# Kernel optimization log

Measured on AMD Instinct MI355X. Metric: run time of the kernel, lower is better.

Reference implementation:

```python
import jax, jax.numpy as jnp
import numpy as np

NUM_TERMS = 3
HIDDEN = 64
CLAMP_MIN = 1e-10


def _hermite_basis(x, num_terms):
    hs = [jnp.ones_like(x)]
    if num_terms > 1:
        hs.append(2.0 * x)
    for n in range(1, num_terms - 1):
        hs.append(2.0 * x * hs[n] - 2.0 * n * hs[n - 1])
    return jnp.stack(hs[:num_terms], axis=-1)  # (..., num_terms)


def setup_inputs() -> dict:
    key = jax.random.key(0)
    ks = jax.random.split(key, 7)
    B, S = 2048, 1024
    ys_coeffs = jax.random.normal(ks[0], (B, S, 2), dtype=jnp.float32)
    # scoring MLP params: Linear(3,64) -> ReLU -> Linear(64,64) -> ReLU -> Linear(64,num_terms)
    def lin(k, fan_in, fan_out):
        bound = 1.0 / np.sqrt(fan_in)
        kw, kb = jax.random.split(k)
        W = jax.random.uniform(kw, (fan_in, fan_out), minval=-bound, maxval=bound, dtype=jnp.float32)
        b = jax.random.uniform(kb, (fan_out,), minval=-bound, maxval=bound, dtype=jnp.float32)
        return W, b
    W1, b1 = lin(ks[1], 3, HIDDEN)
    W2, b2 = lin(ks[2], HIDDEN, HIDDEN)
    Wout, bout = lin(ks[3], HIDDEN, NUM_TERMS)
    return {"ys_coeffs": ys_coeffs, "W1": W1, "b1": b1, "W2": W2, "b2": b2,
            "Wout": Wout, "bout": bout}


def reference(ys_coeffs, W1, b1, W2, b2, Wout, bout):
    B, S, _ = ys_coeffs.shape
    timestamps = ys_coeffs[:, :, 0]
    values = ys_coeffs[:, :, 1]
    x0 = values[:, :-1]            # (B, S-1)
    xt = values[:, 1:]             # (B, S-1)
    t = timestamps[:, 1:]          # (B, S-1)
    feats = jnp.stack([xt, t, x0], axis=-1)           # (B, S-1, 3)
    h1 = jax.nn.relu(feats @ W1 + b1)                 # (B, S-1, 64)
    h2 = jax.nn.relu(h1 @ W2 + b2)                    # (B, S-1, 64)
    c_n = h2 @ Wout + bout                            # (B, S-1, num_terms)
    herm = _hermite_basis(xt, NUM_TERMS)              # (B, S-1, num_terms)
    p = jnp.sum(c_n * herm, axis=-1)                  # (B, S-1)
    p = jax.nn.softmax(p, axis=0)                     # softmax over batch dim (as in torch dim=0)
    log_likelihood = jnp.log(jnp.clip(p, CLAMP_MIN)).sum(axis=-1)  # (B,)
    return log_likelihood.mean()
```

## Files before the change

kernel.cpp:

```cpp
#include <hip/hip_runtime.h>
#include <hip/hip_bf16.h>

#define HIDDEN 64
#define BATCH 2048
#define SFULL 1024
#define SM1 1023
#define LN_CLAMP -23.025850929940457f
#define SP_PER 16

typedef __bf16 bf16x8 __attribute__((ext_vector_type(8)));
typedef float  f32x4  __attribute__((ext_vector_type(4)));

#define FRAG_UNITS 19

__device__ __forceinline__ int permrow(int rho) {
    return 32 * ((rho >> 4) >> 1) + 8 * ((rho >> 2) & 3) + 4 * ((rho >> 4) & 1) + (rho & 3);
}

__device__ __forceinline__ unsigned pkt(float lo, float hi) {
    return __builtin_amdgcn_perm(__float_as_uint(hi), __float_as_uint(lo), 0x07060302u);
}
typedef short s16x2 __attribute__((ext_vector_type(2)));
__device__ __forceinline__ unsigned rp(unsigned x) {
    s16x2 v = __builtin_bit_cast(s16x2, x);
    s16x2 z = {0, 0};
    v = __builtin_elementwise_max(v, z);
    return __builtin_bit_cast(unsigned, v);
}

__device__ __forceinline__ bf16x8 relu_pack2(const f32x4 a, const f32x4 b) {
    union { unsigned u[4]; bf16x8 v; } r;
    r.u[0] = rp(pkt(a[0], a[1]));
    r.u[1] = rp(pkt(a[2], a[3]));
    r.u[2] = rp(pkt(b[0], b[1]));
    r.u[3] = rp(pkt(b[2], b[3]));
    return r.v;
}

__device__ __forceinline__ bf16x8 featpk(float xt, float t, float x0) {
    union { unsigned u[4]; bf16x8 v; } r;
    r.u[0] = pkt(xt, t);
    r.u[1] = pkt(x0, 1.0f);
    r.u[2] = r.u[0]; r.u[3] = r.u[1];
    return r.v;
}

__global__ __launch_bounds__(256) void frag_setup_kernel(
    const float* __restrict__ W1, const float* __restrict__ b1,
    const float* __restrict__ W2, const float* __restrict__ b2,
    const float* __restrict__ Wout, const float* __restrict__ bout,
    char* __restrict__ F)
{
    const int lane = threadIdx.x & 63;
    const int wv   = threadIdx.x >> 6;
    const int col  = lane & 15;
    const int g    = lane >> 4;

    if (wv == 0) {
#pragma unroll
        for (int mt = 0; mt < 4; ++mt) {
            const int p2 = permrow(16 * mt + col);
            bf16x8 v;
#pragma unroll
            for (int j = 0; j < 8; ++j) {
                const int k = 8 * g + j;
                v[j] = (k < 3) ? (__bf16)W1[k * 64 + p2]
                     : (k == 3) ? (__bf16)b1[p2] : (__bf16)0.0f;
            }
            *(bf16x8*)(F + ((mt * 64 + lane) << 4)) = v;
        }
#pragma unroll
        for (int c = 0; c < 2; ++c) {
            bf16x8 v;
#pragma unroll
            for (int j = 0; j < 8; ++j)
                v[j] = (col < 3) ? (__bf16)Wout[(32 * c + 8 * g + j) * 3 + col] : (__bf16)0.0f;
            *(bf16x8*)(F + (((12 + c) * 64 + lane) << 4)) = v;
        }
        f32x4 c3 = {0.f, 0.f, 0.f, 0.f};
        if (g == 0) { c3[0] = bout[0]; c3[1] = bout[1]; c3[2] = bout[2]; }
        *(f32x4*)(F + ((18 * 64 + lane) << 4)) = c3;
    } else if (wv == 1 || wv == 2) {
#pragma unroll
        for (int m = 0; m < 2; ++m) {
            const int mt = (wv - 1) * 2 + m;
            const int p2 = permrow(16 * mt + col);
#pragma unroll
            for (int c = 0; c < 2; ++c) {
                bf16x8 v;
#pragma unroll
                for (int j = 0; j < 8; ++j)
                    v[j] = (__bf16)W2[(32 * c + 8 * g + j) * 64 + p2];
                *(bf16x8*)(F + (((4 + mt * 2 + c) * 64 + lane) << 4)) = v;
            }
        }
    } else {
#pragma unroll
        for (int mt = 0; mt < 4; ++mt) {
            f32x4 v;
#pragma unroll
            for (int r = 0; r < 4; ++r)
                v[r] = b2[permrow(16 * mt + 4 * g + r)];
            *(f32x4*)(F + (((14 + mt) * 64 + lane) << 4)) = v;
        }
    }
}

__global__ __launch_bounds__(256, 4) void mlp_z_kernel(
    const float* __restrict__ ys,
    const char* __restrict__ F,
    float* __restrict__ z)
{
    __shared__ __align__(16) char Flds[14 * 64 * 16];

    const int l    = threadIdx.x & 63;
    const int wv   = threadIdx.x >> 6;
    const int col  = l & 15;

    for (int i = threadIdx.x; i < 14 * 64; i += 256)
        *(f32x4*)(Flds + ((size_t)i << 4)) = *(const f32x4*)(F + ((size_t)i << 4));

    const int b   = (blockIdx.x * 4 + wv) * 16 + col;
    const int sp0 = blockIdx.y * SP_PER;
    const int omax = (SFULL - 1) - sp0;

    f32x4 c2init[4], c3init;
#pragma unroll
    for (int mt = 0; mt < 4; ++mt)
        c2init[mt] = *(const f32x4*)(F + (((14 + mt) * 64 + l) << 4));
    c3init = *(const f32x4*)(F + ((18 * 64 + l) << 4));

    const f32x4 zero4 = {0.f, 0.f, 0.f, 0.f};

    const float2* base2 = reinterpret_cast<const float2*>(ys) + ((size_t)b * SFULL + sp0);
    float* zb = z + (size_t)sp0 * BATCH + b;

    float2 q0 = base2[0];
    float2 q1 = base2[min(1, omax)];
    float2 qn = base2[min(2, omax)];

    __syncthreads();

    for (int it = 0; it < SP_PER; ++it) {
        unsigned loff = (unsigned)(l << 4);
        asm volatile("" : "+v"(loff));
#define LDSF(u) (*(const bf16x8*)(Flds + ((u) * 1024) + loff))

        const float2 qn2 = base2[min(it + 3, omax)];

        const float x0 = q0.y, t = q1.x, xt = q1.y;
        const bf16x8 f0 = featpk(xt, t, x0);

        bf16x8 w10 = LDSF(0), w11 = LDSF(1), w12 = LDSF(2), w13 = LDSF(3);
        f32x4 acc1[4];
        acc1[0] = __builtin_amdgcn_mfma_f32_16x16x32_bf16(w10, f0, zero4, 0, 0, 0);
        acc1[1] = __builtin_amdgcn_mfma_f32_16x16x32_bf16(w11, f0, zero4, 0, 0, 0);
        acc1[2] = __builtin_amdgcn_mfma_f32_16x16x32_bf16(w12, f0, zero4, 0, 0, 0);
        acc1[3] = __builtin_amdgcn_mfma_f32_16x16x32_bf16(w13, f0, zero4, 0, 0, 0);

        bf16x8 w200 = LDSF(4), w210 = LDSF(6), w220 = LDSF(8), w230 = LDSF(10);

        bf16x8 hf[2];
        hf[0] = relu_pack2(acc1[0], acc1[1]);
        hf[1] = relu_pack2(acc1[2], acc1[3]);

        f32x4 acc2[4];
        acc2[0] = __builtin_amdgcn_mfma_f32_16x16x32_bf16(w200, hf[0], c2init[0], 0, 0, 0);
        acc2[1] = __builtin_amdgcn_mfma_f32_16x16x32_bf16(w210, hf[0], c2init[1], 0, 0, 0);
        acc2[2] = __builtin_amdgcn_mfma_f32_16x16x32_bf16(w220, hf[0], c2init[2], 0, 0, 0);
        acc2[3] = __builtin_amdgcn_mfma_f32_16x16x32_bf16(w230, hf[0], c2init[3], 0, 0, 0);

        bf16x8 w201 = LDSF(5), w211 = LDSF(7), w221 = LDSF(9), w231 = LDSF(11);
        acc2[0] = __builtin_amdgcn_mfma_f32_16x16x32_bf16(w201, hf[1], acc2[0], 0, 0, 0);
        acc2[1] = __builtin_amdgcn_mfma_f32_16x16x32_bf16(w211, hf[1], acc2[1], 0, 0, 0);
        acc2[2] = __builtin_amdgcn_mfma_f32_16x16x32_bf16(w221, hf[1], acc2[2], 0, 0, 0);
        acc2[3] = __builtin_amdgcn_mfma_f32_16x16x32_bf16(w231, hf[1], acc2[3], 0, 0, 0);

        bf16x8 w30 = LDSF(12), w31 = LDSF(13);

        bf16x8 h2f[2];
        h2f[0] = relu_pack2(acc2[0], acc2[1]);
        h2f[1] = relu_pack2(acc2[2], acc2[3]);

        f32x4 acc3;
        acc3 = __builtin_amdgcn_mfma_f32_16x16x32_bf16(w30, h2f[0], c3init, 0, 0, 0);
        acc3 = __builtin_amdgcn_mfma_f32_16x16x32_bf16(w31, h2f[1], acc3, 0, 0, 0);
#undef LDSF

        const float zv = fmaf(acc3[2], fmaf(4.0f * xt, xt, -2.0f),
                         fmaf(acc3[1], xt + xt, acc3[0]));

        if (l < 16 && sp0 + it < SM1)
            zb[(size_t)it * BATCH] = zv;

        q0 = q1; q1 = qn; qn = qn2;
    }
}

__device__ __forceinline__ float blk_reduce_max(float v) {
    __shared__ float s[4];
#pragma unroll
    for (int off = 32; off >= 1; off >>= 1) v = fmaxf(v, __shfl_xor(v, off));
    if ((threadIdx.x & 63) == 0) s[threadIdx.x >> 6] = v;
    __syncthreads();
    v = fmaxf(fmaxf(s[0], s[1]), fmaxf(s[2], s[3]));
    __syncthreads();
    return v;
}

__device__ __forceinline__ float blk_reduce_sum(float v) {
    __shared__ float s[4];
#pragma unroll
    for (int off = 32; off >= 1; off >>= 1) v += __shfl_xor(v, off);
    if ((threadIdx.x & 63) == 0) s[threadIdx.x >> 6] = v;
    __syncthreads();
    v = (s[0] + s[1]) + (s[2] + s[3]);
    __syncthreads();
    return v;
}

__global__ __launch_bounds__(256) void col_softmax_kernel(
    const float* __restrict__ z, float* __restrict__ colsum)
{
    const int sp = blockIdx.x;
    const int tid = threadIdx.x;
    const float* col = z + (size_t)sp * BATCH;

    float vals[8];
    float m = -3.4e38f;
#pragma unroll
    for (int i = 0; i < 8; ++i) {
        vals[i] = col[tid + 256 * i];
        m = fmaxf(m, vals[i]);
    }
    const float M = blk_reduce_max(m);

    float se = 0.0f;
#pragma unroll
    for (int i = 0; i < 8; ++i) se += __expf(vals[i] - M);
    const float S = blk_reduce_sum(se);
    const float L = __logf(S);

    float acc = 0.0f;
#pragma unroll
    for (int i = 0; i < 8; ++i) acc += fmaxf(vals[i] - M - L, LN_CLAMP);
    const float T = blk_reduce_sum(acc);
    if (tid == 0) colsum[sp] = T;
}

__global__ __launch_bounds__(256) void final_reduce_kernel(
    const float* __restrict__ colsum, float* __restrict__ out)
{
    const int tid = threadIdx.x;
    float v = 0.0f;
    for (int i = tid; i < SM1; i += 256) v += colsum[i];
    const float T = blk_reduce_sum(v);
    if (tid == 0) out[0] = T / (float)BATCH;
}

extern "C" void kernel_launch(void* const* d_in, const int* in_sizes, int n_in,
                              void* d_out, int out_size, void* d_ws, size_t ws_size,
                              hipStream_t stream) {
    const float* ys   = (const float*)d_in[0];
    const float* W1   = (const float*)d_in[1];
    const float* b1   = (const float*)d_in[2];
    const float* W2   = (const float*)d_in[3];
    const float* b2   = (const float*)d_in[4];
    const float* Wout = (const float*)d_in[5];
    const float* bout = (const float*)d_in[6];
    float* out = (float*)d_out;

    float* z      = (float*)d_ws;
    float* colsum = z + (size_t)SM1 * BATCH;
    size_t fo = ((size_t)SM1 * BATCH + SM1) * sizeof(float);
    fo = (fo + 15) & ~(size_t)15;
    char* F = (char*)d_ws + fo;

    frag_setup_kernel<<<1, 256, 0, stream>>>(W1, b1, W2, b2, Wout, bout, F);
    dim3 grid1(32, 64);
    mlp_z_kernel<<<grid1, 256, 0, stream>>>(ys, F, z);
    col_softmax_kernel<<<SM1, 256, 0, stream>>>(z, colsum);
    final_reduce_kernel<<<1, 256, 0, stream>>>(colsum, out);
}
```

Before: 45.45 us.

## Keep MLP weight fragments in registers instead of LDS, parallelize fragment setup

The MLP kernel now loads all weight fragments (W1, W2, Wout) into registers once per thread, which removes the LDS staging copy, the block barrier and the per-iteration LDS reads. Launch bounds drop from 4 to 3 blocks per SIMD/CU to allow the extra VGPRs. The fragment setup kernel is split across 19 single-wave blocks so each fragment unit is built in parallel. The cost is higher register pressure and lower occupancy, which may reduce latency hiding for the global loads of ys.

New measurement: 43.87 us. -3.5%, faster.

```diff
diff --git a/kernel.cpp b/kernel.cpp
--- a/kernel.cpp
+++ b/kernel.cpp
@@ -10,6 +10,7 @@
 
 typedef __bf16 bf16x8 __attribute__((ext_vector_type(8)));
 typedef float  f32x4  __attribute__((ext_vector_type(4)));
+typedef short  s16x2  __attribute__((ext_vector_type(2)));
 
 #define FRAG_UNITS 19
 
@@ -20,7 +21,6 @@
 __device__ __forceinline__ unsigned pkt(float lo, float hi) {
     return __builtin_amdgcn_perm(__float_as_uint(hi), __float_as_uint(lo), 0x07060302u);
 }
-typedef short s16x2 __attribute__((ext_vector_type(2)));
 __device__ __forceinline__ unsigned rp(unsigned x) {
     s16x2 v = __builtin_bit_cast(s16x2, x);
     s16x2 z = {0, 0};
@@ -45,89 +45,81 @@
     return r.v;
 }
 
-__global__ __launch_bounds__(256) void frag_setup_kernel(
+__global__ __launch_bounds__(64) void frag_setup_kernel(
     const float* __restrict__ W1, const float* __restrict__ b1,
     const float* __restrict__ W2, const float* __restrict__ b2,
     const float* __restrict__ Wout, const float* __restrict__ bout,
     char* __restrict__ F)
 {
-    const int lane = threadIdx.x & 63;
-    const int wv   = threadIdx.x >> 6;
-    const int col  = lane & 15;
-    const int g    = lane >> 4;
-
-    if (wv == 0) {
-#pragma unroll
-        for (int mt = 0; mt < 4; ++mt) {
-            const int p2 = permrow(16 * mt + col);
-            bf16x8 v;
-#pragma unroll
-            for (int j = 0; j < 8; ++j) {
-                const int k = 8 * g + j;
-                v[j] = (k < 3) ? (__bf16)W1[k * 64 + p2]
-                     : (k == 3) ? (__bf16)b1[p2] : (__bf16)0.0f;
-            }
-            *(bf16x8*)(F + ((mt * 64 + lane) << 4)) = v;
+    const int l   = threadIdx.x;
+    const int u   = blockIdx.x;
+    const int col = l & 15;
+    const int g   = l >> 4;
+
+    if (u < 4) {
+        const int p2 = permrow(16 * u + col);
+        bf16x8 v;
+#pragma unroll
+        for (int j = 0; j < 8; ++j) {
+            const int k = 8 * g + j;
+            v[j] = (k < 3) ? (__bf16)W1[k * 64 + p2]
+                 : (k == 3) ? (__bf16)b1[p2] : (__bf16)0.0f;
         }
-#pragma unroll
-        for (int c = 0; c < 2; ++c) {
-            bf16x8 v;
-#pragma unroll
-            for (int j = 0; j < 8; ++j)
-                v[j] = (col < 3) ? (__bf16)Wout[(32 * c + 8 * g + j) * 3 + col] : (__bf16)0.0f;
-            *(bf16x8*)(F + (((12 + c) * 64 + lane) << 4)) = v;
-        }
-        f32x4 c3 = {0.f, 0.f, 0.f, 0.f};
-        if (g == 0) { c3[0] = bout[0]; c3[1] = bout[1]; c3[2] = bout[2]; }
-        *(f32x4*)(F + ((18 * 64 + lane) << 4)) = c3;
-    } else if (wv == 1 || wv == 2) {
-#pragma unroll
-        for (int m = 0; m < 2; ++m) {
-            const int mt = (wv - 1) * 2 + m;
-            const int p2 = permrow(16 * mt + col);
-#pragma unroll
-            for (int c = 0; c < 2; ++c) {
-                bf16x8 v;
-#pragma unroll
-                for (int j = 0; j < 8; ++j)
-                    v[j] = (__bf16)W2[(32 * c + 8 * g + j) * 64 + p2];
-                *(bf16x8*)(F + (((4 + mt * 2 + c) * 64 + lane) << 4)) = v;
-            }
-        }
+        *(bf16x8*)(F + ((u * 64 + l) << 4)) = v;
+    } else if (u < 12) {
+        const int mt = (u - 4) >> 1;
+        const int c  = (u - 4) & 1;
+        const int p2 = permrow(16 * mt + col);
+        bf16x8 v;
+#pragma unroll
+        for (int j = 0; j < 8; ++j)
+            v[j] = (__bf16)W2[(32 * c + 8 * g + j) * 64 + p2];
+        *(bf16x8*)(F + ((u * 64 + l) << 4)) = v;
+    } else if (u < 14) {
+        const int c = u - 12;
+        bf16x8 v;
+#pragma unroll
+        for (int j = 0; j < 8; ++j)
+            v[j] = (col < 3) ? (__bf16)Wout[(32 * c + 8 * g + j) * 3 + col] : (__bf16)0.0f;
+        *(bf16x8*)(F + ((u * 64 + l) << 4)) = v;
+    } else if (u < 18) {
+        const int mt = u - 14;
+        f32x4 v;
+#pragma unroll
+        for (int r = 0; r < 4; ++r)
+            v[r] = b2[permrow(16 * mt + 4 * g + r)];
+        *(f32x4*)(F + ((u * 64 + l) << 4)) = v;
     } else {
-#pragma unroll
-        for (int mt = 0; mt < 4; ++mt) {
-            f32x4 v;
-#pragma unroll
-            for (int r = 0; r < 4; ++r)
-                v[r] = b2[permrow(16 * mt + 4 * g + r)];
-            *(f32x4*)(F + (((14 + mt) * 64 + lane) << 4)) = v;
-        }
-    }
-}
-
-__global__ __launch_bounds__(256, 4) void mlp_z_kernel(
+        f32x4 v = {0.f, 0.f, 0.f, 0.f};
+        if (g == 0) { v[0] = bout[0]; v[1] = bout[1]; v[2] = bout[2]; }
+        *(f32x4*)(F + ((u * 64 + l) << 4)) = v;
+    }
+}
+
+__global__ __launch_bounds__(256, 3) void mlp_z_kernel(
     const float* __restrict__ ys,
     const char* __restrict__ F,
     float* __restrict__ z)
 {
-    __shared__ __align__(16) char Flds[14 * 64 * 16];
-
-    const int l    = threadIdx.x & 63;
-    const int wv   = threadIdx.x >> 6;
-    const int col  = l & 15;
-
-    for (int i = threadIdx.x; i < 14 * 64; i += 256)
-        *(f32x4*)(Flds + ((size_t)i << 4)) = *(const f32x4*)(F + ((size_t)i << 4));
+    const int l   = threadIdx.x & 63;
+    const int wv  = threadIdx.x >> 6;
+    const int col = l & 15;
 
     const int b   = (blockIdx.x * 4 + wv) * 16 + col;
     const int sp0 = blockIdx.y * SP_PER;
     const int omax = (SFULL - 1) - sp0;
 
+    bf16x8 a1[4], a2[4][2], a3[2];
     f32x4 c2init[4], c3init;
 #pragma unroll
-    for (int mt = 0; mt < 4; ++mt)
+    for (int mt = 0; mt < 4; ++mt) {
+        a1[mt]     = *(const bf16x8*)(F + ((mt * 64 + l) << 4));
+        a2[mt][0]  = *(const bf16x8*)(F + (((4 + mt * 2) * 64 + l) << 4));
+        a2[mt][1]  = *(const bf16x8*)(F + (((5 + mt * 2) * 64 + l) << 4));
         c2init[mt] = *(const f32x4*)(F + (((14 + mt) * 64 + l) << 4));
+    }
+    a3[0]  = *(const bf16x8*)(F + ((12 * 64 + l) << 4));
+    a3[1]  = *(const bf16x8*)(F + ((13 * 64 + l) << 4));
     c3init = *(const f32x4*)(F + ((18 * 64 + l) << 4));
 
     const f32x4 zero4 = {0.f, 0.f, 0.f, 0.f};
@@ -139,53 +131,39 @@
     float2 q1 = base2[min(1, omax)];
     float2 qn = base2[min(2, omax)];
 
-    __syncthreads();
-
     for (int it = 0; it < SP_PER; ++it) {
-        unsigned loff = (unsigned)(l << 4);
-        asm volatile("" : "+v"(loff));
-#define LDSF(u) (*(const bf16x8*)(Flds + ((u) * 1024) + loff))
-
         const float2 qn2 = base2[min(it + 3, omax)];
 
         const float x0 = q0.y, t = q1.x, xt = q1.y;
         const bf16x8 f0 = featpk(xt, t, x0);
 
-        bf16x8 w10 = LDSF(0), w11 = LDSF(1), w12 = LDSF(2), w13 = LDSF(3);
         f32x4 acc1[4];
-        acc1[0] = __builtin_amdgcn_mfma_f32_16x16x32_bf16(w10, f0, zero4, 0, 0, 0);
-        acc1[1] = __builtin_amdgcn_mfma_f32_16x16x32_bf16(w11, f0, zero4, 0, 0, 0);
-        acc1[2] = __builtin_amdgcn_mfma_f32_16x16x32_bf16(w12, f0, zero4, 0, 0, 0);
-        acc1[3] = __builtin_amdgcn_mfma_f32_16x16x32_bf16(w13, f0, zero4, 0, 0, 0);
-
-        bf16x8 w200 = LDSF(4), w210 = LDSF(6), w220 = LDSF(8), w230 = LDSF(10);
+        acc1[0] = __builtin_amdgcn_mfma_f32_16x16x32_bf16(a1[0], f0, zero4, 0, 0, 0);
+        acc1[1] = __builtin_amdgcn_mfma_f32_16x16x32_bf16(a1[1], f0, zero4, 0, 0, 0);
+        acc1[2] = __builtin_amdgcn_mfma_f32_16x16x32_bf16(a1[2], f0, zero4, 0, 0, 0);
+        acc1[3] = __builtin_amdgcn_mfma_f32_16x16x32_bf16(a1[3], f0, zero4, 0, 0, 0);
 
         bf16x8 hf[2];
         hf[0] = relu_pack2(acc1[0], acc1[1]);
         hf[1] = relu_pack2(acc1[2], acc1[3]);
 
         f32x4 acc2[4];
-        acc2[0] = __builtin_amdgcn_mfma_f32_16x16x32_bf16(w200, hf[0], c2init[0], 0, 0, 0);
-        acc2[1] = __builtin_amdgcn_mfma_f32_16x16x32_bf16(w210, hf[0], c2init[1], 0, 0, 0);
-        acc2[2] = __builtin_amdgcn_mfma_f32_16x16x32_bf16(w220, hf[0], c2init[2], 0, 0, 0);
-        acc2[3] = __builtin_amdgcn_mfma_f32_16x16x32_bf16(w230, hf[0], c2init[3], 0, 0, 0);
-
-        bf16x8 w201 = LDSF(5), w211 = LDSF(7), w221 = LDSF(9), w231 = LDSF(11);
-        acc2[0] = __builtin_amdgcn_mfma_f32_16x16x32_bf16(w201, hf[1], acc2[0], 0, 0, 0);
-        acc2[1] = __builtin_amdgcn_mfma_f32_16x16x32_bf16(w211, hf[1], acc2[1], 0, 0, 0);
-        acc2[2] = __builtin_amdgcn_mfma_f32_16x16x32_bf16(w221, hf[1], acc2[2], 0, 0, 0);
-        acc2[3] = __builtin_amdgcn_mfma_f32_16x16x32_bf16(w231, hf[1], acc2[3], 0, 0, 0);
-
-        bf16x8 w30 = LDSF(12), w31 = LDSF(13);
+        acc2[0] = __builtin_amdgcn_mfma_f32_16x16x32_bf16(a2[0][0], hf[0], c2init[0], 0, 0, 0);
+        acc2[1] = __builtin_amdgcn_mfma_f32_16x16x32_bf16(a2[1][0], hf[0], c2init[1], 0, 0, 0);
+        acc2[2] = __builtin_amdgcn_mfma_f32_16x16x32_bf16(a2[2][0], hf[0], c2init[2], 0, 0, 0);
+        acc2[3] = __builtin_amdgcn_mfma_f32_16x16x32_bf16(a2[3][0], hf[0], c2init[3], 0, 0, 0);
+        acc2[0] = __builtin_amdgcn_mfma_f32_16x16x32_bf16(a2[0][1], hf[1], acc2[0], 0, 0, 0);
+        acc2[1] = __builtin_amdgcn_mfma_f32_16x16x32_bf16(a2[1][1], hf[1], acc2[1], 0, 0, 0);
+        acc2[2] = __builtin_amdgcn_mfma_f32_16x16x32_bf16(a2[2][1], hf[1], acc2[2], 0, 0, 0);
+        acc2[3] = __builtin_amdgcn_mfma_f32_16x16x32_bf16(a2[3][1], hf[1], acc2[3], 0, 0, 0);
 
         bf16x8 h2f[2];
         h2f[0] = relu_pack2(acc2[0], acc2[1]);
         h2f[1] = relu_pack2(acc2[2], acc2[3]);
 
         f32x4 acc3;
-        acc3 = __builtin_amdgcn_mfma_f32_16x16x32_bf16(w30, h2f[0], c3init, 0, 0, 0);
-        acc3 = __builtin_amdgcn_mfma_f32_16x16x32_bf16(w31, h2f[1], acc3, 0, 0, 0);
-#undef LDSF
+        acc3 = __builtin_amdgcn_mfma_f32_16x16x32_bf16(a3[0], h2f[0], c3init, 0, 0, 0);
+        acc3 = __builtin_amdgcn_mfma_f32_16x16x32_bf16(a3[1], h2f[1], acc3, 0, 0, 0);
 
         const float zv = fmaf(acc3[2], fmaf(4.0f * xt, xt, -2.0f),
                          fmaf(acc3[1], xt + xt, acc3[0]));
@@ -276,7 +254,7 @@
     fo = (fo + 15) & ~(size_t)15;
     char* F = (char*)d_ws + fo;
 
-    frag_setup_kernel<<<1, 256, 0, stream>>>(W1, b1, W2, b2, Wout, bout, F);
+    frag_setup_kernel<<<FRAG_UNITS, 64, 0, stream>>>(W1, b1, W2, b2, Wout, bout, F);
     dim3 grid1(32, 64);
     mlp_z_kernel<<<grid1, 256, 0, stream>>>(ys, F, z);
     col_softmax_kernel<<<SM1, 256, 0, stream>>>(z, colsum);
```
